# Performance work log

Measured on AMD Instinct MI355X. Metric: run time of the kernel, lower is better.

The kernel has to match this reference:

```python
import jax, jax.numpy as jnp
import numpy as np

BATCH = 8192          # per-modality batch size; n = 2*BATCH
FEAT = 128            # feature dim (kept small -> memory-bound n^2 distance matrix)
NUM_IDS = 1000
MARGIN = 0.3


def setup_inputs() -> dict:
    key = jax.random.key(0)
    k1, k2 = jax.random.split(key)
    n = 2 * BATCH
    inputs = jax.random.normal(k1, (n, FEAT), dtype=jnp.float32)
    # same identity set in both modality halves -> cross-modal positives exist per row
    t = jax.random.randint(k2, (BATCH,), 0, NUM_IDS, dtype=jnp.int32)
    targets = jnp.concatenate([t, t], axis=0)
    return {"inputs": inputs, "targets": targets}


def reference(inputs, targets):
    n = inputs.shape[0]
    # pairwise euclidean distances: ||xi||^2 + ||xj||^2 - 2 xi.xj
    sq = jnp.sum(inputs * inputs, axis=1)                      # [n]
    d2 = sq[:, None] + sq[None, :] - 2.0 * (inputs @ inputs.T)  # [n, n]
    dist = jnp.sqrt(jnp.clip(d2, 1e-12, None))
    # modality: first half 0, second half 1; self.sub selects CROSS-modality pairs
    modality = jnp.arange(n) >= (n // 2)
    cross = modality[:, None] != modality[None, :]              # [n, n] bool
    same = targets[:, None] == targets[None, :]                 # same identity
    pos = same & cross        # mask1: same label, different modality
    neg = (~same) & cross     # mask2: diff label, different modality
    # masked hard mining: per-row max over positives, min over negatives
    dist_ap = jnp.max(jnp.where(pos, dist, -jnp.inf), axis=1)   # [n]
    dist_an = jnp.min(jnp.where(neg, dist, jnp.inf), axis=1)    # [n]
    # MarginRankingLoss with y=1: mean(relu(-(dist_an - dist_ap) + margin))
    loss = jnp.mean(jax.nn.relu(dist_ap - dist_an + MARGIN))
    correct = jnp.sum(dist_an >= dist_ap).astype(jnp.int32)
    return (loss, correct)
```

## Files before the change

### kernel.cpp

```cpp
#include <hip/hip_runtime.h>

#define N_TOTAL 16384
#define HALF    8192
#define FEAT    128
#define MARGIN  0.3f
#define NBINS   1024

typedef __attribute__((ext_vector_type(8))) short  short8v;
typedef __attribute__((ext_vector_type(4))) float  float4v;

__device__ __forceinline__ unsigned short f32_to_bf16_rne(float f) {
    unsigned u = __float_as_uint(f);
    u += 0x7FFFu + ((u >> 16) & 1u);
    return (unsigned short)(u >> 16);
}

__global__ __launch_bounds__(1024) void sort_init_kernel(
        const int* __restrict__ targets, int* __restrict__ cursor,
        int* __restrict__ accs ) {
    __shared__ int lhist[2 * NBINS];
    const int t = threadIdx.x;
    lhist[t] = 0; lhist[NBINS + t] = 0;
    __syncthreads();
    #pragma unroll
    for (int k = 0; k < 16; ++k) {
        int i = k * 1024 + t;
        int h = i >> 13;
        atomicAdd(&lhist[(h << 10) + targets[i]], 1);
    }
    __syncthreads();
    const int lane = t & 63, wave = t >> 6;
    int x0 = lhist[t], x1 = lhist[NBINS + t];
    const int o0 = x0, o1 = x1;
    #pragma unroll
    for (int m = 1; m < 64; m <<= 1) {
        int v0 = __shfl_up(x0, m, 64);
        int v1 = __shfl_up(x1, m, 64);
        if (lane >= m) { x0 += v0; x1 += v1; }
    }
    __shared__ int wsum[32];
    if (lane == 63) { wsum[wave] = x0; wsum[16 + wave] = x1; }
    __syncthreads();
    if (t == 0) {
        int s = 0;
        for (int w = 0; w < 16; ++w)  { int v = wsum[w]; wsum[w] = s; s += v; }
        s = 0;
        for (int w = 16; w < 32; ++w) { int v = wsum[w]; wsum[w] = s; s += v; }
        accs[0] = 0; accs[1] = 0; accs[2] = 0;
    }
    __syncthreads();
    cursor[t]         = x0 - o0 + wsum[wave];
    cursor[NBINS + t] = x1 - o1 + wsum[16 + wave];
}

__global__ __launch_bounds__(256) void prep_kernel(
        const float* __restrict__ X, const int* __restrict__ targets,
        int* __restrict__ cursor,
        unsigned* __restrict__ Xb, float* __restrict__ sq, int* __restrict__ labs,
        int* __restrict__ maxpos, int* __restrict__ minneg) {
    const int wave = threadIdx.x >> 6, lane = threadIdx.x & 63;
    const int src = blockIdx.x * 4 + wave;
    const int h   = src >> 13;
    const int lbl = targets[src];
    int dst;
    if (lane == 0)
        dst = (h << 13) + atomicAdd(&cursor[(h << 10) + lbl], 1);
    dst = __shfl(dst, 0, 64);
    const float2 xv = ((const float2*)(X + (size_t)src * FEAT))[lane];
    unsigned short h0 = f32_to_bf16_rne(xv.x);
    unsigned short h1 = f32_to_bf16_rne(xv.y);
    Xb[dst * 64 + lane] = (unsigned)h0 | ((unsigned)h1 << 16);
    float x0 = __uint_as_float((unsigned)h0 << 16);
    float x1 = __uint_as_float((unsigned)h1 << 16);
    float p = x0 * x0 + x1 * x1;
    #pragma unroll
    for (int m = 1; m < 64; m <<= 1) p += __shfl_xor(p, m, 64);
    if (lane == 0) {
        sq[dst]     = p;
        labs[dst]   = lbl;
        maxpos[dst] = (int)0xFF800000u;
        minneg[dst] = 0x7F800000;
    }
}

__global__ __launch_bounds__(512, 4) void cross_kernel(
        const unsigned short* __restrict__ Xb, const float* __restrict__ sq,
        const int* __restrict__ labs,
        int* __restrict__ maxpos, int* __restrict__ minneg) {
    __shared__ unsigned short As[128 * 128];
    __shared__ unsigned short Bs[128 * 128];
    const int bm = blockIdx.x, bn = blockIdx.y;
    const int t  = threadIdx.x;

    const unsigned short* Ag = Xb + (size_t)bm * 128 * FEAT;
    const unsigned short* Bg = Xb + (size_t)(HALF + bn * 128) * FEAT;
    #pragma unroll
    for (int p = 0; p < 4; ++p) {
        int idx = p * 512 + t;
        int row = idx >> 4, ch = idx & 15;
        int sc  = ch ^ (row & 7);
        uint4 va = ((const uint4*)Ag)[idx];
        uint4 vb = ((const uint4*)Bg)[idx];
        *(uint4*)&As[row * 128 + sc * 8] = va;
        *(uint4*)&Bs[row * 128 + sc * 8] = vb;
    }
    __syncthreads();

    const int wave = t >> 6, lane = t & 63;
    const int q = lane >> 4, c = lane & 15;
    const int wr = (wave >> 1) * 32;
    const int wc = (wave & 1) * 64;

    float4v acc[2][4] = {};
    #pragma unroll
    for (int kk = 0; kk < 4; ++kk) {
        short8v af[2], bfr[4];
        #pragma unroll
        for (int ti = 0; ti < 2; ++ti) {
            int row = wr + ti * 16 + c;
            int sc  = (kk * 4 + q) ^ (row & 7);
            af[ti] = *(const short8v*)&As[row * 128 + sc * 8];
        }
        #pragma unroll
        for (int tj = 0; tj < 4; ++tj) {
            int row = wc + tj * 16 + c;
            int sc  = (kk * 4 + q) ^ (row & 7);
            bfr[tj] = *(const short8v*)&Bs[row * 128 + sc * 8];
        }
        #pragma unroll
        for (int ti = 0; ti < 2; ++ti)
            #pragma unroll
            for (int tj = 0; tj < 4; ++tj)
                acc[ti][tj] = __builtin_amdgcn_mfma_f32_16x16x32_bf16(
                    af[ti], bfr[tj], acc[ti][tj], 0, 0, 0);
    }

    const float NEG_INF = __int_as_float((int)0xFF800000u);
    const float POS_INF = __int_as_float(0x7F800000);

    const int aMin = labs[bm * 128], aMax = labs[bm * 128 + 127];
    const int bMn  = labs[HALF + bn * 128], bMx = labs[HALF + bn * 128 + 127];
    const bool overlap = (aMax >= bMn) && (bMx >= aMin);

    float sA[8];
    #pragma unroll
    for (int ti = 0; ti < 2; ++ti)
        #pragma unroll
        for (int reg = 0; reg < 4; ++reg)
            sA[ti * 4 + reg] = sq[bm * 128 + wr + ti * 16 + q * 4 + reg];
    float sB[4];
    #pragma unroll
    for (int tj = 0; tj < 4; ++tj)
        sB[tj] = sq[HALF + bn * 128 + wc + tj * 16 + c];

    float rmin[8], cmin[4];
    #pragma unroll
    for (int i = 0; i < 8; ++i) rmin[i] = POS_INF;
    #pragma unroll
    for (int j = 0; j < 4; ++j) cmin[j] = POS_INF;

    if (!overlap) {
        #pragma unroll
        for (int ti = 0; ti < 2; ++ti)
            #pragma unroll
            for (int tj = 0; tj < 4; ++tj)
                #pragma unroll
                for (int reg = 0; reg < 4; ++reg) {
                    int ri = ti * 4 + reg;
                    float d2 = fmaf(acc[ti][tj][reg], -2.0f, sA[ri] + sB[tj]);
                    rmin[ri] = fminf(rmin[ri], d2);
                    cmin[tj] = fminf(cmin[tj], d2);
                }
        #pragma unroll
        for (int m = 1; m <= 8; m <<= 1)
            #pragma unroll
            for (int i = 0; i < 8; ++i)
                rmin[i] = fminf(rmin[i], __shfl_xor(rmin[i], m, 64));
        if (c == 0) {
            #pragma unroll
            for (int ti = 0; ti < 2; ++ti)
                #pragma unroll
                for (int reg = 0; reg < 4; ++reg)
                    atomicMin(&minneg[bm * 128 + wr + ti * 16 + q * 4 + reg],
                              __float_as_int(rmin[ti * 4 + reg]));
        }
        #pragma unroll
        for (int m = 16; m <= 32; m <<= 1)
            #pragma unroll
            for (int j = 0; j < 4; ++j)
                cmin[j] = fminf(cmin[j], __shfl_xor(cmin[j], m, 64));
        if (q == 0) {
            #pragma unroll
            for (int tj = 0; tj < 4; ++tj)
                atomicMin(&minneg[HALF + bn * 128 + wc + tj * 16 + c],
                          __float_as_int(cmin[tj]));
        }
    } else {
        float rmax[8], cmax[4];
        #pragma unroll
        for (int i = 0; i < 8; ++i) rmax[i] = NEG_INF;
        #pragma unroll
        for (int j = 0; j < 4; ++j) cmax[j] = NEG_INF;

        int tA[8];
        #pragma unroll
        for (int ti = 0; ti < 2; ++ti)
            #pragma unroll
            for (int reg = 0; reg < 4; ++reg)
                tA[ti * 4 + reg] = labs[bm * 128 + wr + ti * 16 + q * 4 + reg];
        int tB[4];
        #pragma unroll
        for (int tj = 0; tj < 4; ++tj)
            tB[tj] = labs[HALF + bn * 128 + wc + tj * 16 + c];

        #pragma unroll
        for (int ti = 0; ti < 2; ++ti)
            #pragma unroll
            for (int tj = 0; tj < 4; ++tj) {
                #pragma unroll
                for (int reg = 0; reg < 4; ++reg) {
                    int ri = ti * 4 + reg;
                    float d2 = fmaf(acc[ti][tj][reg], -2.0f, sA[ri] + sB[tj]);
                    bool same = (tA[ri] == tB[tj]);
                    float posc = same ? d2 : NEG_INF;
                    float negc = same ? POS_INF : d2;
                    rmax[ri] = fmaxf(rmax[ri], posc);
                    cmax[tj] = fmaxf(cmax[tj], posc);
                    rmin[ri] = fminf(rmin[ri], negc);
                    cmin[tj] = fminf(cmin[tj], negc);
                }
            }
        #pragma unroll
        for (int m = 1; m <= 8; m <<= 1)
            #pragma unroll
            for (int i = 0; i < 8; ++i) {
                rmax[i] = fmaxf(rmax[i], __shfl_xor(rmax[i], m, 64));
                rmin[i] = fminf(rmin[i], __shfl_xor(rmin[i], m, 64));
            }
        if (c == 0) {
            #pragma unroll
            for (int ti = 0; ti < 2; ++ti)
                #pragma unroll
                for (int reg = 0; reg < 4; ++reg) {
                    int gi = bm * 128 + wr + ti * 16 + q * 4 + reg;
                    atomicMax(&maxpos[gi], __float_as_int(rmax[ti * 4 + reg]));
                    atomicMin(&minneg[gi], __float_as_int(rmin[ti * 4 + reg]));
                }
        }
        #pragma unroll
        for (int m = 16; m <= 32; m <<= 1)
            #pragma unroll
            for (int j = 0; j < 4; ++j) {
                cmax[j] = fmaxf(cmax[j], __shfl_xor(cmax[j], m, 64));
                cmin[j] = fminf(cmin[j], __shfl_xor(cmin[j], m, 64));
            }
        if (q == 0) {
            #pragma unroll
            for (int tj = 0; tj < 4; ++tj) {
                int gj = HALF + bn * 128 + wc + tj * 16 + c;
                atomicMax(&maxpos[gj], __float_as_int(cmax[tj]));
                atomicMin(&minneg[gj], __float_as_int(cmin[tj]));
            }
        }
    }
}

__global__ __launch_bounds__(256) void final_kernel(
        const int* __restrict__ maxpos, const int* __restrict__ minneg,
        int* __restrict__ accs ,
        float* __restrict__ out) {
    const int i = blockIdx.x * 256 + threadIdx.x;
    const int t = threadIdx.x;
    float* accF  = (float*)&accs[0];
    int*   accI  = &accs[1];
    int*   tick  = &accs[2];
    float ap = sqrtf(fmaxf(__int_as_float(maxpos[i]), 1e-12f));
    float an = sqrtf(fmaxf(__int_as_float(minneg[i]), 1e-12f));
    float term = fmaxf(ap - an + MARGIN, 0.0f);
    int cnt = (an >= ap) ? 1 : 0;
    #pragma unroll
    for (int m = 1; m < 64; m <<= 1) {
        term += __shfl_xor(term, m, 64);
        cnt  += __shfl_xor(cnt, m, 64);
    }
    __shared__ float sf[4];
    __shared__ int   si[4];
    if ((t & 63) == 0) { sf[t >> 6] = term; si[t >> 6] = cnt; }
    __syncthreads();
    if (t == 0) {
        atomicAdd(accF, sf[0] + sf[1] + sf[2] + sf[3]);
        atomicAdd(accI, si[0] + si[1] + si[2] + si[3]);
        __threadfence();
        int old = atomicAdd(tick, 1);
        if (old == gridDim.x - 1) {
            __threadfence();
            float S = atomicAdd(accF, 0.0f);
            int   C = atomicAdd(accI, 0);
            out[0] = S / (float)N_TOTAL;
            out[1] = (float)C;
        }
    }
}

extern "C" void kernel_launch(void* const* d_in, const int* in_sizes, int n_in,
                              void* d_out, int out_size, void* d_ws, size_t ws_size,
                              hipStream_t stream) {
    const float* X       = (const float*)d_in[0];
    const int*   targets = (const int*)d_in[1];
    float* out = (float*)d_out;

    char* ws = (char*)d_ws;
    const size_t XB_BYTES = (size_t)N_TOTAL * FEAT * 2;
    unsigned* Xb  = (unsigned*)ws;
    float* sq     = (float*)(ws + XB_BYTES);
    int* maxpos   = (int*)(ws + XB_BYTES + 1 * 65536);
    int* minneg   = (int*)(ws + XB_BYTES + 2 * 65536);
    int* labs     = (int*)(ws + XB_BYTES + 3 * 65536);
    int* cursor   = (int*)(ws + XB_BYTES + 4 * 65536);
    int* accs     = cursor + 2 * NBINS;

    sort_init_kernel<<<1, 1024, 0, stream>>>(targets, cursor, accs);
    prep_kernel     <<<4096, 256, 0, stream>>>(X, targets, cursor, Xb, sq, labs,
                                               maxpos, minneg);
    cross_kernel    <<<dim3(64, 64), 512, 0, stream>>>(
        (const unsigned short*)Xb, sq, labs, maxpos, minneg);
    final_kernel    <<<64, 256, 0, stream>>>(maxpos, minneg, accs, out);
}
```

Baseline: 132.7 us.

## Drop LDS staging in cross kernel, use DPP row reductions, split histogram

The cross kernel no longer stages the A/B tiles in shared memory. Each wave now loads its MFMA fragments directly from global memory and computes a 64x64 subtile, with 4 waves per block instead of 8. Intra-row reductions switch from shfl_xor to DPP moves, and the histogram/scan runs as two blocks, one per modality half, instead of one. This removes LDS traffic and barriers, at the cost of more register pressure and redundant global/L2 reads across waves.

```diff
diff --git a/kernel.cpp b/kernel.cpp
--- a/kernel.cpp
+++ b/kernel.cpp
@@ -15,42 +15,57 @@
     return (unsigned short)(u >> 16);
 }
 
-__global__ __launch_bounds__(1024) void sort_init_kernel(
+template<int CTRL>
+__device__ __forceinline__ float dpp_mov_f(float x) {
+    return __int_as_float(__builtin_amdgcn_update_dpp(
+        0, __float_as_int(x), CTRL, 0xF, 0xF, true));
+}
+__device__ __forceinline__ float rowmin16(float x) {
+    x = fminf(x, dpp_mov_f<0xB1>(x));
+    x = fminf(x, dpp_mov_f<0x4E>(x));
+    x = fminf(x, dpp_mov_f<0x141>(x));
+    x = fminf(x, dpp_mov_f<0x140>(x));
+    return x;
+}
+__device__ __forceinline__ float rowmax16(float x) {
+    x = fmaxf(x, dpp_mov_f<0xB1>(x));
+    x = fmaxf(x, dpp_mov_f<0x4E>(x));
+    x = fmaxf(x, dpp_mov_f<0x141>(x));
+    x = fmaxf(x, dpp_mov_f<0x140>(x));
+    return x;
+}
+
+__global__ __launch_bounds__(1024) void histscan_kernel(
         const int* __restrict__ targets, int* __restrict__ cursor,
         int* __restrict__ accs ) {
-    __shared__ int lhist[2 * NBINS];
+    __shared__ int lhist[NBINS];
+    const int h = blockIdx.x;
     const int t = threadIdx.x;
-    lhist[t] = 0; lhist[NBINS + t] = 0;
-    __syncthreads();
-    #pragma unroll
-    for (int k = 0; k < 16; ++k) {
-        int i = k * 1024 + t;
-        int h = i >> 13;
-        atomicAdd(&lhist[(h << 10) + targets[i]], 1);
-    }
+    lhist[t] = 0;
+    __syncthreads();
+    const int* tg = targets + (h << 13);
+    #pragma unroll
+    for (int k = 0; k < 8; ++k)
+        atomicAdd(&lhist[tg[k * 1024 + t]], 1);
     __syncthreads();
     const int lane = t & 63, wave = t >> 6;
-    int x0 = lhist[t], x1 = lhist[NBINS + t];
-    const int o0 = x0, o1 = x1;
+    int x = lhist[t];
+    const int orig = x;
     #pragma unroll
     for (int m = 1; m < 64; m <<= 1) {
-        int v0 = __shfl_up(x0, m, 64);
-        int v1 = __shfl_up(x1, m, 64);
-        if (lane >= m) { x0 += v0; x1 += v1; }
-    }
-    __shared__ int wsum[32];
-    if (lane == 63) { wsum[wave] = x0; wsum[16 + wave] = x1; }
+        int v = __shfl_up(x, m, 64);
+        if (lane >= m) x += v;
+    }
+    __shared__ int wsum[16];
+    if (lane == 63) wsum[wave] = x;
     __syncthreads();
     if (t == 0) {
         int s = 0;
-        for (int w = 0; w < 16; ++w)  { int v = wsum[w]; wsum[w] = s; s += v; }
-        s = 0;
-        for (int w = 16; w < 32; ++w) { int v = wsum[w]; wsum[w] = s; s += v; }
-        accs[0] = 0; accs[1] = 0; accs[2] = 0;
-    }
-    __syncthreads();
-    cursor[t]         = x0 - o0 + wsum[wave];
-    cursor[NBINS + t] = x1 - o1 + wsum[16 + wave];
+        for (int w = 0; w < 16; ++w) { int v = wsum[w]; wsum[w] = s; s += v; }
+        if (h == 0) { accs[0] = 0; accs[1] = 0; accs[2] = 0; }
+    }
+    __syncthreads();
+    cursor[(h << 10) + t] = x - orig + wsum[wave];
 }
 
 __global__ __launch_bounds__(256) void prep_kernel(
@@ -83,52 +98,37 @@
     }
 }
 
-__global__ __launch_bounds__(512, 4) void cross_kernel(
+__global__ __launch_bounds__(256, 3) void cross_kernel(
         const unsigned short* __restrict__ Xb, const float* __restrict__ sq,
         const int* __restrict__ labs,
         int* __restrict__ maxpos, int* __restrict__ minneg) {
-    __shared__ unsigned short As[128 * 128];
-    __shared__ unsigned short Bs[128 * 128];
     const int bm = blockIdx.x, bn = blockIdx.y;
     const int t  = threadIdx.x;
-
-    const unsigned short* Ag = Xb + (size_t)bm * 128 * FEAT;
-    const unsigned short* Bg = Xb + (size_t)(HALF + bn * 128) * FEAT;
-    #pragma unroll
-    for (int p = 0; p < 4; ++p) {
-        int idx = p * 512 + t;
-        int row = idx >> 4, ch = idx & 15;
-        int sc  = ch ^ (row & 7);
-        uint4 va = ((const uint4*)Ag)[idx];
-        uint4 vb = ((const uint4*)Bg)[idx];
-        *(uint4*)&As[row * 128 + sc * 8] = va;
-        *(uint4*)&Bs[row * 128 + sc * 8] = vb;
-    }
-    __syncthreads();
-
     const int wave = t >> 6, lane = t & 63;
     const int q = lane >> 4, c = lane & 15;
-    const int wr = (wave >> 1) * 32;
-    const int wc = (wave & 1) * 64;
-
-    float4v acc[2][4] = {};
+    const int wr = (wave >> 1) * 64, wc = (wave & 1) * 64;
+
+    const unsigned short* pA[4];
+    const unsigned short* pB[4];
+    #pragma unroll
+    for (int ti = 0; ti < 4; ++ti)
+        pA[ti] = Xb + (size_t)(bm * 128 + wr + ti * 16 + c) * FEAT + q * 8;
+    #pragma unroll
+    for (int tj = 0; tj < 4; ++tj)
+        pB[tj] = Xb + (size_t)(HALF + bn * 128 + wc + tj * 16 + c) * FEAT + q * 8;
+
+    float4v acc[4][4] = {};
     #pragma unroll
     for (int kk = 0; kk < 4; ++kk) {
-        short8v af[2], bfr[4];
-        #pragma unroll
-        for (int ti = 0; ti < 2; ++ti) {
-            int row = wr + ti * 16 + c;
-            int sc  = (kk * 4 + q) ^ (row & 7);
-            af[ti] = *(const short8v*)&As[row * 128 + sc * 8];
-        }
-        #pragma unroll
-        for (int tj = 0; tj < 4; ++tj) {
-            int row = wc + tj * 16 + c;
-            int sc  = (kk * 4 + q) ^ (row & 7);
-            bfr[tj] = *(const short8v*)&Bs[row * 128 + sc * 8];
-        }
-        #pragma unroll
-        for (int ti = 0; ti < 2; ++ti)
+        short8v af[4], bfr[4];
+        #pragma unroll
+        for (int ti = 0; ti < 4; ++ti)
+            af[ti] = *(const short8v*)(pA[ti] + kk * 32);
+        #pragma unroll
+        for (int tj = 0; tj < 4; ++tj)
+            bfr[tj] = *(const short8v*)(pB[tj] + kk * 32);
+        #pragma unroll
+        for (int ti = 0; ti < 4; ++ti)
             #pragma unroll
             for (int tj = 0; tj < 4; ++tj)
                 acc[ti][tj] = __builtin_amdgcn_mfma_f32_16x16x32_bf16(
@@ -142,9 +142,9 @@
     const int bMn  = labs[HALF + bn * 128], bMx = labs[HALF + bn * 128 + 127];
     const bool overlap = (aMax >= bMn) && (bMx >= aMin);
 
-    float sA[8];
-    #pragma unroll
-    for (int ti = 0; ti < 2; ++ti)
+    float sA[16];
+    #pragma unroll
+    for (int ti = 0; ti < 4; ++ti)
         #pragma unroll
         for (int reg = 0; reg < 4; ++reg)
             sA[ti * 4 + reg] = sq[bm * 128 + wr + ti * 16 + q * 4 + reg];
@@ -153,15 +153,15 @@
     for (int tj = 0; tj < 4; ++tj)
         sB[tj] = sq[HALF + bn * 128 + wc + tj * 16 + c];
 
-    float rmin[8], cmin[4];
-    #pragma unroll
-    for (int i = 0; i < 8; ++i) rmin[i] = POS_INF;
-    #pragma unroll
-    for (int j = 0; j < 4; ++j) cmin[j] = POS_INF;
+    float rmin[16], cmin[4];
+    #pragma unroll
+    for (int i = 0; i < 16; ++i) rmin[i] = POS_INF;
+    #pragma unroll
+    for (int j = 0; j < 4; ++j)  cmin[j] = POS_INF;
 
     if (!overlap) {
         #pragma unroll
-        for (int ti = 0; ti < 2; ++ti)
+        for (int ti = 0; ti < 4; ++ti)
             #pragma unroll
             for (int tj = 0; tj < 4; ++tj)
                 #pragma unroll
@@ -172,13 +172,10 @@
                     cmin[tj] = fminf(cmin[tj], d2);
                 }
         #pragma unroll
-        for (int m = 1; m <= 8; m <<= 1)
-            #pragma unroll
-            for (int i = 0; i < 8; ++i)
-                rmin[i] = fminf(rmin[i], __shfl_xor(rmin[i], m, 64));
+        for (int i = 0; i < 16; ++i) rmin[i] = rowmin16(rmin[i]);
         if (c == 0) {
             #pragma unroll
-            for (int ti = 0; ti < 2; ++ti)
+            for (int ti = 0; ti < 4; ++ti)
                 #pragma unroll
                 for (int reg = 0; reg < 4; ++reg)
                     atomicMin(&minneg[bm * 128 + wr + ti * 16 + q * 4 + reg],
@@ -196,15 +193,15 @@
                           __float_as_int(cmin[tj]));
         }
     } else {
-        float rmax[8], cmax[4];
-        #pragma unroll
-        for (int i = 0; i < 8; ++i) rmax[i] = NEG_INF;
-        #pragma unroll
-        for (int j = 0; j < 4; ++j) cmax[j] = NEG_INF;
-
-        int tA[8];
-        #pragma unroll
-        for (int ti = 0; ti < 2; ++ti)
+        float rmax[16], cmax[4];
+        #pragma unroll
+        for (int i = 0; i < 16; ++i) rmax[i] = NEG_INF;
+        #pragma unroll
+        for (int j = 0; j < 4; ++j)  cmax[j] = NEG_INF;
+
+        int tA[16];
+        #pragma unroll
+        for (int ti = 0; ti < 4; ++ti)
             #pragma unroll
             for (int reg = 0; reg < 4; ++reg)
                 tA[ti * 4 + reg] = labs[bm * 128 + wr + ti * 16 + q * 4 + reg];
@@ -214,7 +211,7 @@
             tB[tj] = labs[HALF + bn * 128 + wc + tj * 16 + c];
 
         #pragma unroll
-        for (int ti = 0; ti < 2; ++ti)
+        for (int ti = 0; ti < 4; ++ti)
             #pragma unroll
             for (int tj = 0; tj < 4; ++tj) {
                 #pragma unroll
@@ -231,15 +228,13 @@
                 }
             }
         #pragma unroll
-        for (int m = 1; m <= 8; m <<= 1)
-            #pragma unroll
-            for (int i = 0; i < 8; ++i) {
-                rmax[i] = fmaxf(rmax[i], __shfl_xor(rmax[i], m, 64));
-                rmin[i] = fminf(rmin[i], __shfl_xor(rmin[i], m, 64));
-            }
+        for (int i = 0; i < 16; ++i) {
+            rmax[i] = rowmax16(rmax[i]);
+            rmin[i] = rowmin16(rmin[i]);
+        }
         if (c == 0) {
             #pragma unroll
-            for (int ti = 0; ti < 2; ++ti)
+            for (int ti = 0; ti < 4; ++ti)
                 #pragma unroll
                 for (int reg = 0; reg < 4; ++reg) {
                     int gi = bm * 128 + wr + ti * 16 + q * 4 + reg;
@@ -319,10 +314,10 @@
     int* cursor   = (int*)(ws + XB_BYTES + 4 * 65536);
     int* accs     = cursor + 2 * NBINS;
 
-    sort_init_kernel<<<1, 1024, 0, stream>>>(targets, cursor, accs);
-    prep_kernel     <<<4096, 256, 0, stream>>>(X, targets, cursor, Xb, sq, labs,
-                                               maxpos, minneg);
-    cross_kernel    <<<dim3(64, 64), 512, 0, stream>>>(
+    histscan_kernel<<<2, 1024, 0, stream>>>(targets, cursor, accs);
+    prep_kernel    <<<4096, 256, 0, stream>>>(X, targets, cursor, Xb, sq, labs,
+                                              maxpos, minneg);
+    cross_kernel   <<<dim3(64, 64), 256, 0, stream>>>(
         (const unsigned short*)Xb, sq, labs, maxpos, minneg);
-    final_kernel    <<<64, 256, 0, stream>>>(maxpos, minneg, accs, out);
-}
+    final_kernel   <<<64, 256, 0, stream>>>(maxpos, minneg, accs, out);
+}
```

New measurement: 159.3 us. 1.2x slower.
